# Optimization experiments

Hardware: AMD Instinct MI355X
Metric: run time of the kernel (lower is better)

## Reference

```python
import jax, jax.numpy as jnp
import numpy as np

B, C_IN, L, NCLASS = 256, 6, 512, 10

def setup_inputs() -> dict:
    key = jax.random.key(0)
    ks = jax.random.split(key, 16)
    g = lambda k, shp, s=0.05: jax.random.normal(k, shp, dtype=jnp.float32) * s
    return {
        "x": jax.random.normal(ks[0], (B, C_IN, L), dtype=jnp.float32),
        "conv1_w": g(ks[1], (32, C_IN, 3)),
        "conv1_b": g(ks[2], (32,)),
        "bn1_g": jnp.ones((32,), jnp.float32),
        "bn1_b": jnp.zeros((32,), jnp.float32),
        "bn1_m": g(ks[3], (32,)),
        "bn1_v": jnp.abs(g(ks[4], (32,))) + 1.0,
        "conv2_w": g(ks[5], (64, 32, 3)),
        "conv2_b": g(ks[6], (64,)),
        "bn2_g": jnp.ones((64,), jnp.float32),
        "bn2_b": jnp.zeros((64,), jnp.float32),
        "bn2_m": g(ks[7], (64,)),
        "bn2_v": jnp.abs(g(ks[8], (64,))) + 1.0,
        "wq": g(ks[9], (64, 64)),
        "bq": g(ks[10], (64,)),
        "wk": g(ks[11], (64, 64)),
        "bk": g(ks[12], (64,)),
        "wv": g(ks[13], (64, 64)),
        "bv": g(ks[14], (64,)),
        "fc_w": g(ks[15], (NCLASS, 64)),
        "fc_b": jnp.zeros((NCLASS,), jnp.float32),
    }

def _conv1d(x, w, b):
    # x: [B, C, L], w: [O, C, 3], padding=1 -> same length
    y = jax.lax.conv_general_dilated(
        x, w, window_strides=(1,), padding=[(1, 1)],
        dimension_numbers=("NCH", "OIH", "NCH"))
    return y + b[None, :, None]

def _bn(x, g, b, m, v, eps=1e-5):
    # eval-mode BatchNorm1d over channel dim of [B, C, L]
    inv = g * jax.lax.rsqrt(v + eps)
    return x * inv[None, :, None] + (b - m * inv)[None, :, None]

def reference(x, conv1_w, conv1_b, bn1_g, bn1_b, bn1_m, bn1_v,
              conv2_w, conv2_b, bn2_g, bn2_b, bn2_m, bn2_v,
              wq, bq, wk, bk, wv, bv, fc_w, fc_b):
    h = jax.nn.relu(_bn(_conv1d(x, conv1_w, conv1_b), bn1_g, bn1_b, bn1_m, bn1_v))
    h = jax.nn.relu(_bn(_conv1d(h, conv2_w, conv2_b), bn2_g, bn2_b, bn2_m, bn2_v))
    h = h.transpose(0, 2, 1)                      # [B, L, 64]
    q = h @ wq.T + bq
    k = h @ wk.T + bk
    v = h @ wv.T + bv
    scores = jnp.einsum("bqd,bkd->bqk", q, k) / jnp.sqrt(jnp.float32(64.0))
    attn = jax.nn.softmax(scores, axis=-1)
    out = jnp.einsum("bqk,bkd->bqd", attn, v)     # [B, L, 64]
    pooled = out.mean(axis=1)                     # [B, 64]
    return pooled @ fc_w.T + fc_b                 # [B, n_class]
```

## Files before the change

### kernel.cpp

```cpp
#include <hip/hip_runtime.h>
#include <hip/hip_bf16.h>


#define NB 256
#define LL 512
#define CIN 6
#define NCLASS 10
#define SLAB 8192
#define QSC 0.18033688f

typedef __bf16 bf16x8 __attribute__((ext_vector_type(8)));
typedef float f32x4 __attribute__((ext_vector_type(4)));
typedef unsigned short us4 __attribute__((ext_vector_type(4)));
typedef unsigned short us8 __attribute__((ext_vector_type(8)));
typedef unsigned int u32x4 __attribute__((ext_vector_type(4)));

static __device__ __forceinline__ unsigned short f2b(float f) {
    __bf16 h = (__bf16)f;
    return __builtin_bit_cast(unsigned short, h);
}

__global__ __launch_bounds__(256) void prep_weights(
    const float* __restrict__ w1, const float* __restrict__ cb1,
    const float* __restrict__ g1, const float* __restrict__ be1,
    const float* __restrict__ m1, const float* __restrict__ v1,
    const float* __restrict__ w2, const float* __restrict__ cb2,
    const float* __restrict__ g2, const float* __restrict__ be2,
    const float* __restrict__ m2, const float* __restrict__ v2,
    const float* __restrict__ wq, const float* __restrict__ wk,
    const float* __restrict__ wv,
    unsigned short* __restrict__ w1p, float* __restrict__ b1f,
    unsigned short* __restrict__ w2p, float* __restrict__ b2f,
    unsigned short* __restrict__ wqp, unsigned short* __restrict__ wkp,
    unsigned short* __restrict__ wvp)
{
    const int t = threadIdx.x;
    for (int idx = t; idx < 1024; idx += 256) {
        int c = idx >> 5, k = idx & 31;
        int dl = k >> 3, ci = k & 7;
        float inv = g1[c] * rsqrtf(v1[c] + 1e-5f);
        float val = (dl < 3 && ci < 6) ? w1[c * 18 + ci * 3 + dl] * inv : 0.f;
        w1p[idx] = f2b(val);
    }
    if (t < 32) {
        float inv = g1[t] * rsqrtf(v1[t] + 1e-5f);
        b1f[t] = be1[t] + (cb1[t] - m1[t]) * inv;
    }
    for (int idx = t; idx < 2048; idx += 256) {
        int c2 = idx >> 5, ci = idx & 31;
        float inv = g2[c2] * rsqrtf(v2[c2] + 1e-5f);
        const float* wp = w2 + c2 * 96 + ci * 3;
        w2p[c2 * 96 +      ci] = f2b(wp[0] * inv);
        w2p[c2 * 96 + 32 + ci] = f2b(wp[1] * inv);
        w2p[c2 * 96 + 64 + ci] = f2b(wp[2] * inv);
    }
    if (t >= 64 && t < 128) {
        int c2 = t - 64;
        float inv = g2[c2] * rsqrtf(v2[c2] + 1e-5f);
        b2f[c2] = be2[c2] + (cb2[c2] - m2[c2]) * inv;
    }
    for (int idx = t; idx < 4096; idx += 256) {
        int d = idx >> 6, k = idx & 63;
        int kc = k >> 5, quad = (k >> 3) & 3, e = k & 7;
        int ch = kc * 32 + (e >> 2) * 16 + quad * 4 + (e & 3);
        wqp[idx] = f2b(wq[d * 64 + ch] * QSC);
        wkp[idx] = f2b(wk[d * 64 + ch]);
        wvp[idx] = f2b(wv[d * 64 + ch]);
    }
}

__global__ __launch_bounds__(1024, 4) void fused_all(
    const float* __restrict__ x,
    const unsigned short* __restrict__ w1p, const float* __restrict__ b1f,
    const unsigned short* __restrict__ w2p, const float* __restrict__ b2f,
    const unsigned short* __restrict__ wqp, const unsigned short* __restrict__ wkp,
    const unsigned short* __restrict__ wvp,
    const float* __restrict__ bq, const float* __restrict__ bk,
    const float* __restrict__ bvp,
    const float* __restrict__ fcw, const float* __restrict__ fcb,
    float* __restrict__ outp)
{
    const int b = blockIdx.x;
    const int t = threadIdx.x;
    const int w = t >> 6, lane = t & 63, quad = lane >> 4, lc = lane & 15;

    __shared__ __align__(16) char smem[16 * SLAB + 8192];
    char* myslab = smem + w * SLAB;
    unsigned short* h1sl = (unsigned short*)myslab;
    unsigned short* Kf   = (unsigned short*)myslab;
    unsigned short* Vf   = (unsigned short*)(myslab + 4096);
    unsigned short* xstage = (unsigned short*)(smem + 16 * SLAB);
    float* redw   = (float*)(smem + 16 * SLAB) + w * 64;
    float* pooled = (float*)(smem + 16 * SLAB + 4096);

    if (t < 512) {
        us8 pk;
        #pragma unroll
        for (int ci = 0; ci < 6; ci++)
            pk[ci] = f2b(x[((size_t)b * CIN + ci) * LL + t]);
        pk[6] = 0; pk[7] = 0;
        *(us8*)&xstage[t * 8] = pk;
    }
    __syncthreads();

    bf16x8 bW1[2];
    #pragma unroll
    for (int nt = 0; nt < 2; nt++)
        bW1[nt] = *(const bf16x8*)(w1p + (nt * 16 + lc) * 32 + quad * 8);
    f32x4 b1q[2];
    #pragma unroll
    for (int nt = 0; nt < 2; nt++)
        b1q[nt] = *(const f32x4*)&b1f[nt * 16 + quad * 4];
    #pragma unroll
    for (int mt = 0; mt < 3; mt++) {
        int j = mt * 16 + lc;
        int P = w * 32 - 1 + j;
        int src = P + quad - 1;
        bool okx = (src >= 0) && (src < LL);
        int srcc = src < 0 ? 0 : (src > 511 ? 511 : src);
        u32x4 xv = *(const u32x4*)&xstage[srcc * 8];
        if (!okx) { xv[0] = 0u; xv[1] = 0u; xv[2] = 0u; xv[3] = 0u; }
        bf16x8 aX = __builtin_bit_cast(bf16x8, xv);
        bool pv = (P >= 0) && (P < LL);
        #pragma unroll
        for (int nt = 0; nt < 2; nt++) {
            f32x4 z = {0.f, 0.f, 0.f, 0.f};
            f32x4 h = __builtin_amdgcn_mfma_f32_16x16x32_bf16(bW1[nt], aX, z, 0, 0, 0);
            us4 pk;
            #pragma unroll
            for (int r = 0; r < 4; r++) {
                float y = h[r] + b1q[nt][r];
                y = (pv && y > 0.f) ? y : 0.f;
                pk[r] = f2b(y);
            }
            if (j < 34)
                *(us4*)&h1sl[j * 40 + nt * 16 + quad * 4] = pk;
        }
    }

    bf16x8 bX[2][3], aW2[4][3];
    #pragma unroll
    for (int rt = 0; rt < 2; rt++)
        #pragma unroll
        for (int kc = 0; kc < 3; kc++)
            bX[rt][kc] = *(const bf16x8*)&h1sl[(rt * 16 + lc + kc) * 40 + quad * 8];
    #pragma unroll
    for (int nt = 0; nt < 4; nt++)
        #pragma unroll
        for (int kc = 0; kc < 3; kc++)
            aW2[nt][kc] = *(const bf16x8*)(w2p + (nt * 16 + lc) * 96 + kc * 32 + quad * 8);

    f32x4 acc2[4][2];
    #pragma unroll
    for (int nt = 0; nt < 4; nt++)
        #pragma unroll
        for (int rt = 0; rt < 2; rt++) {
            f32x4 a = {0.f, 0.f, 0.f, 0.f};
            a = __builtin_amdgcn_mfma_f32_16x16x32_bf16(aW2[nt][0], bX[rt][0], a, 0, 0, 0);
            a = __builtin_amdgcn_mfma_f32_16x16x32_bf16(aW2[nt][1], bX[rt][1], a, 0, 0, 0);
            acc2[nt][rt] = __builtin_amdgcn_mfma_f32_16x16x32_bf16(aW2[nt][2], bX[rt][2], a, 0, 0, 0);
        }

    bf16x8 aH[2][2];
    #pragma unroll
    for (int nt2 = 0; nt2 < 4; nt2++) {
        f32x4 bb2 = *(const f32x4*)&b2f[nt2 * 16 + quad * 4];
        #pragma unroll
        for (int rt = 0; rt < 2; rt++)
            #pragma unroll
            for (int reg = 0; reg < 4; reg++) {
                float y = acc2[nt2][rt][reg] + bb2[reg];
                aH[rt][nt2 >> 1][(nt2 & 1) * 4 + reg] = (__bf16)(y > 0.f ? y : 0.f);
            }
    }

    bf16x8 aQ[2][2];
    {
        f32x4 Cq[4][2], bbq[4];
        #pragma unroll
        for (int nt = 0; nt < 4; nt++) {
            bf16x8 aW0 = *(const bf16x8*)(wqp + (nt * 16 + lc) * 64 + quad * 8);
            bf16x8 aW1 = *(const bf16x8*)(wqp + (nt * 16 + lc) * 64 + 32 + quad * 8);
            bbq[nt] = *(const f32x4*)&bq[nt * 16 + quad * 4];
            #pragma unroll
            for (int rt = 0; rt < 2; rt++) {
                f32x4 a = {0.f, 0.f, 0.f, 0.f};
                a = __builtin_amdgcn_mfma_f32_16x16x32_bf16(aW0, aH[rt][0], a, 0, 0, 0);
                Cq[nt][rt] = __builtin_amdgcn_mfma_f32_16x16x32_bf16(aW1, aH[rt][1], a, 0, 0, 0);
            }
        }
        #pragma unroll
        for (int rt = 0; rt < 2; rt++)
            #pragma unroll
            for (int nt = 0; nt < 4; nt++)
                #pragma unroll
                for (int reg = 0; reg < 4; reg++)
                    aQ[rt][nt >> 1][(nt & 1) * 4 + reg] =
                        (__bf16)(Cq[nt][rt][reg] + bbq[nt][reg] * QSC);
    }
    {
        f32x4 Ck[4][2], bbk[4];
        #pragma unroll
        for (int nt = 0; nt < 4; nt++) {
            bf16x8 aW0 = *(const bf16x8*)(wkp + (nt * 16 + lc) * 64 + quad * 8);
            bf16x8 aW1 = *(const bf16x8*)(wkp + (nt * 16 + lc) * 64 + 32 + quad * 8);
            bbk[nt] = *(const f32x4*)&bk[nt * 16 + quad * 4];
            #pragma unroll
            for (int rt = 0; rt < 2; rt++) {
                f32x4 a = {0.f, 0.f, 0.f, 0.f};
                a = __builtin_amdgcn_mfma_f32_16x16x32_bf16(aW0, aH[rt][0], a, 0, 0, 0);
                Ck[nt][rt] = __builtin_amdgcn_mfma_f32_16x16x32_bf16(aW1, aH[rt][1], a, 0, 0, 0);
            }
        }
        #pragma unroll
        for (int rt = 0; rt < 2; rt++)
            #pragma unroll
            for (int kc = 0; kc < 2; kc++) {
                us8 pk;
                #pragma unroll
                for (int e = 0; e < 8; e++) {
                    int nt = kc * 2 + (e >> 2), reg = e & 3;
                    pk[e] = f2b(Ck[nt][rt][reg] + bbk[nt][reg]);
                }
                *(us8*)&Kf[((rt * 2 + kc) << 9) + lane * 8] = pk;
            }
    }

    #pragma unroll
    for (int nt = 0; nt < 4; nt++) {
        bf16x8 bW0 = *(const bf16x8*)(wvp + (nt * 16 + lc) * 64 + quad * 8);
        bf16x8 bW1 = *(const bf16x8*)(wvp + (nt * 16 + lc) * 64 + 32 + quad * 8);
        const float bvv = bvp[nt * 16 + lc];
        f32x4 a0, a1;
        {
            f32x4 z = {0.f, 0.f, 0.f, 0.f};
            z = __builtin_amdgcn_mfma_f32_16x16x32_bf16(aH[0][0], bW0, z, 0, 0, 0);
            a0 = __builtin_amdgcn_mfma_f32_16x16x32_bf16(aH[0][1], bW1, z, 0, 0, 0);
        }
        {
            f32x4 z = {0.f, 0.f, 0.f, 0.f};
            z = __builtin_amdgcn_mfma_f32_16x16x32_bf16(aH[1][0], bW0, z, 0, 0, 0);
            a1 = __builtin_amdgcn_mfma_f32_16x16x32_bf16(aH[1][1], bW1, z, 0, 0, 0);
        }
        us8 pk;
        #pragma unroll
        for (int reg = 0; reg < 4; reg++) {
            pk[reg]     = f2b(a0[reg] + bvv);
            pk[4 + reg] = f2b(a1[reg] + bvv);
        }
        *(us8*)&Vf[nt * 512 + lane * 8] = pk;
    }

    __syncthreads();

    f32x4 outacc[2][4];
    #pragma unroll
    for (int rt = 0; rt < 2; rt++)
        #pragma unroll
        for (int dt = 0; dt < 4; dt++) outacc[rt][dt] = (f32x4){0.f, 0.f, 0.f, 0.f};
    float den[2] = {0.f, 0.f};

    bf16x8 bK2[2][2];
    {
        const unsigned short* sK = (const unsigned short*)smem;
        #pragma unroll
        for (int nt = 0; nt < 2; nt++)
            #pragma unroll
            for (int kc = 0; kc < 2; kc++)
                bK2[nt][kc] = *(const bf16x8*)&sK[((nt * 2 + kc) << 9) + lane * 8];
    }
    f32x4 sv[2][2];
    #pragma unroll
    for (int nt = 0; nt < 2; nt++)
        #pragma unroll
        for (int rt = 0; rt < 2; rt++) {
            f32x4 z = {0.f, 0.f, 0.f, 0.f};
            z = __builtin_amdgcn_mfma_f32_16x16x32_bf16(bK2[nt][0], aQ[rt][0], z, 0, 0, 0);
            sv[nt][rt] = __builtin_amdgcn_mfma_f32_16x16x32_bf16(bK2[nt][1], aQ[rt][1], z, 0, 0, 0);
        }

    for (int cc = 0; cc < 16; cc++) {
        const unsigned short* sV = (const unsigned short*)(smem + cc * SLAB + 4096);
        bf16x8 bV[4];
        #pragma unroll
        for (int dt = 0; dt < 4; dt++)
            bV[dt] = *(const bf16x8*)&sV[dt * 512 + lane * 8];
        if (cc < 15) {
            const unsigned short* sKn = (const unsigned short*)(smem + (cc + 1) * SLAB);
            #pragma unroll
            for (int nt = 0; nt < 2; nt++)
                #pragma unroll
                for (int kc = 0; kc < 2; kc++)
                    bK2[nt][kc] = *(const bf16x8*)&sKn[((nt * 2 + kc) << 9) + lane * 8];
        }
        bf16x8 aP[2];
        #pragma unroll
        for (int rt = 0; rt < 2; rt++)
            #pragma unroll
            for (int nt = 0; nt < 2; nt++)
                #pragma unroll
                for (int reg = 0; reg < 4; reg++) {
                    float p = __builtin_amdgcn_exp2f(sv[nt][rt][reg]);
                    den[rt] += p;
                    aP[rt][nt * 4 + reg] = (__bf16)p;
                }
        __builtin_amdgcn_s_setprio(1);
        #pragma unroll
        for (int dt = 0; dt < 4; dt++) {
            outacc[0][dt] = __builtin_amdgcn_mfma_f32_16x16x32_bf16(aP[0], bV[dt], outacc[0][dt], 0, 0, 0);
            outacc[1][dt] = __builtin_amdgcn_mfma_f32_16x16x32_bf16(aP[1], bV[dt], outacc[1][dt], 0, 0, 0);
        }
        if (cc < 15) {
            #pragma unroll
            for (int nt = 0; nt < 2; nt++)
                #pragma unroll
                for (int rt = 0; rt < 2; rt++) {
                    f32x4 z = {0.f, 0.f, 0.f, 0.f};
                    z = __builtin_amdgcn_mfma_f32_16x16x32_bf16(bK2[nt][0], aQ[rt][0], z, 0, 0, 0);
                    sv[nt][rt] = __builtin_amdgcn_mfma_f32_16x16x32_bf16(bK2[nt][1], aQ[rt][1], z, 0, 0, 0);
                }
        }
        __builtin_amdgcn_s_setprio(0);
    }

    float rden[2][4];
    #pragma unroll
    for (int rt = 0; rt < 2; rt++) {
        float d2 = den[rt];
        d2 += __shfl_xor(d2, 16);
        d2 += __shfl_xor(d2, 32);
        d2 = 1.0f / d2;
        #pragma unroll
        for (int reg = 0; reg < 4; reg++)
            rden[rt][reg] = __shfl(d2, quad * 4 + reg);
    }
    #pragma unroll
    for (int dt = 0; dt < 4; dt++) {
        float ps = 0.f;
        #pragma unroll
        for (int rt = 0; rt < 2; rt++)
            #pragma unroll
            for (int reg = 0; reg < 4; reg++)
                ps += outacc[rt][dt][reg] * rden[rt][reg];
        ps += __shfl_xor(ps, 16);
        ps += __shfl_xor(ps, 32);
        if (quad == 0) redw[dt * 16 + lc] = ps;
    }
    __syncthreads();
    if (t < 64) {
        float s = 0.f;
        #pragma unroll
        for (int ww = 0; ww < 16; ww++)
            s += *(const float*)(smem + 16 * SLAB + ww * 256 + t * 4);
        pooled[t] = s * (1.0f / 512.0f);
    }
    __syncthreads();
    if (t < NCLASS) {
        float acc = fcb[t];
        #pragma unroll
        for (int d = 0; d < 64; d++) acc += pooled[d] * fcw[t * 64 + d];
        outp[b * NCLASS + t] = acc;
    }
}

extern "C" void kernel_launch(void* const* d_in, const int* in_sizes, int n_in,
                              void* d_out, int out_size, void* d_ws, size_t ws_size,
                              hipStream_t stream)
{
    const float* x   = (const float*)d_in[0];
    const float* w1  = (const float*)d_in[1];
    const float* cb1 = (const float*)d_in[2];
    const float* g1  = (const float*)d_in[3];
    const float* be1 = (const float*)d_in[4];
    const float* m1  = (const float*)d_in[5];
    const float* v1  = (const float*)d_in[6];
    const float* w2  = (const float*)d_in[7];
    const float* cb2 = (const float*)d_in[8];
    const float* g2  = (const float*)d_in[9];
    const float* be2 = (const float*)d_in[10];
    const float* m2  = (const float*)d_in[11];
    const float* v2  = (const float*)d_in[12];
    const float* wq  = (const float*)d_in[13];
    const float* bq  = (const float*)d_in[14];
    const float* wk  = (const float*)d_in[15];
    const float* bk  = (const float*)d_in[16];
    const float* wv  = (const float*)d_in[17];
    const float* bv  = (const float*)d_in[18];
    const float* fcw = (const float*)d_in[19];
    const float* fcb = (const float*)d_in[20];
    float* out = (float*)d_out;

    char* ws = (char*)d_ws;
    unsigned short* w1p = (unsigned short*)(ws);
    float*          b1f = (float*)(ws + 2048u);
    float*          b2f = (float*)(ws + 2176u);
    unsigned short* w2p = (unsigned short*)(ws + 2432u);
    unsigned short* wqp = (unsigned short*)(ws + 14720u);
    unsigned short* wkp = (unsigned short*)(ws + 22912u);
    unsigned short* wvp = (unsigned short*)(ws + 31104u);

    prep_weights<<<dim3(1), 256, 0, stream>>>(w1, cb1, g1, be1, m1, v1,
                                              w2, cb2, g2, be2, m2, v2,
                                              wq, wk, wv,
                                              w1p, b1f, w2p, b2f, wqp, wkp, wvp);
    fused_all<<<dim3(NB), 1024, 0, stream>>>(x, w1p, b1f, w2p, b2f,
                                             wqp, wkp, wvp,
                                             bq, bk, bv, fcw, fcb, out);
}
```

Baseline: 130.0 us.

## Halve block to 512 threads with each wave owning two query tiles

```diff
diff --git a/kernel.cpp b/kernel.cpp
--- a/kernel.cpp
+++ b/kernel.cpp
@@ -34,19 +34,19 @@
     unsigned short* __restrict__ wqp, unsigned short* __restrict__ wkp,
     unsigned short* __restrict__ wvp)
 {
-    const int t = threadIdx.x;
-    for (int idx = t; idx < 1024; idx += 256) {
+    const int tt = blockIdx.x * 256 + threadIdx.x;
+    for (int idx = tt; idx < 1024; idx += 2048) {
         int c = idx >> 5, k = idx & 31;
         int dl = k >> 3, ci = k & 7;
         float inv = g1[c] * rsqrtf(v1[c] + 1e-5f);
         float val = (dl < 3 && ci < 6) ? w1[c * 18 + ci * 3 + dl] * inv : 0.f;
         w1p[idx] = f2b(val);
     }
-    if (t < 32) {
-        float inv = g1[t] * rsqrtf(v1[t] + 1e-5f);
-        b1f[t] = be1[t] + (cb1[t] - m1[t]) * inv;
-    }
-    for (int idx = t; idx < 2048; idx += 256) {
+    if (tt < 32) {
+        float inv = g1[tt] * rsqrtf(v1[tt] + 1e-5f);
+        b1f[tt] = be1[tt] + (cb1[tt] - m1[tt]) * inv;
+    }
+    for (int idx = tt; idx < 2048; idx += 2048) {
         int c2 = idx >> 5, ci = idx & 31;
         float inv = g2[c2] * rsqrtf(v2[c2] + 1e-5f);
         const float* wp = w2 + c2 * 96 + ci * 3;
@@ -54,12 +54,12 @@
         w2p[c2 * 96 + 32 + ci] = f2b(wp[1] * inv);
         w2p[c2 * 96 + 64 + ci] = f2b(wp[2] * inv);
     }
-    if (t >= 64 && t < 128) {
-        int c2 = t - 64;
+    if (tt >= 64 && tt < 128) {
+        int c2 = tt - 64;
         float inv = g2[c2] * rsqrtf(v2[c2] + 1e-5f);
         b2f[c2] = be2[c2] + (cb2[c2] - m2[c2]) * inv;
     }
-    for (int idx = t; idx < 4096; idx += 256) {
+    for (int idx = tt; idx < 4096; idx += 2048) {
         int d = idx >> 6, k = idx & 63;
         int kc = k >> 5, quad = (k >> 3) & 3, e = k & 7;
         int ch = kc * 32 + (e >> 2) * 16 + quad * 4 + (e & 3);
@@ -69,7 +69,7 @@
     }
 }
 
-__global__ __launch_bounds__(1024, 4) void fused_all(
+__global__ __launch_bounds__(512, 2) void fused_all(
     const float* __restrict__ x,
     const unsigned short* __restrict__ w1p, const float* __restrict__ b1f,
     const unsigned short* __restrict__ w2p, const float* __restrict__ b2f,
@@ -85,15 +85,11 @@
     const int w = t >> 6, lane = t & 63, quad = lane >> 4, lc = lane & 15;
 
     __shared__ __align__(16) char smem[16 * SLAB + 8192];
-    char* myslab = smem + w * SLAB;
-    unsigned short* h1sl = (unsigned short*)myslab;
-    unsigned short* Kf   = (unsigned short*)myslab;
-    unsigned short* Vf   = (unsigned short*)(myslab + 4096);
     unsigned short* xstage = (unsigned short*)(smem + 16 * SLAB);
     float* redw   = (float*)(smem + 16 * SLAB) + w * 64;
     float* pooled = (float*)(smem + 16 * SLAB + 4096);
 
-    if (t < 512) {
+    {
         us8 pk;
         #pragma unroll
         for (int ci = 0; ci < 6; ci++)
@@ -103,162 +99,171 @@
     }
     __syncthreads();
 
-    bf16x8 bW1[2];
+    bf16x8 aQ4[4][2];
     #pragma unroll
-    for (int nt = 0; nt < 2; nt++)
-        bW1[nt] = *(const bf16x8*)(w1p + (nt * 16 + lc) * 32 + quad * 8);
-    f32x4 b1q[2];
-    #pragma unroll
-    for (int nt = 0; nt < 2; nt++)
-        b1q[nt] = *(const f32x4*)&b1f[nt * 16 + quad * 4];
-    #pragma unroll
-    for (int mt = 0; mt < 3; mt++) {
-        int j = mt * 16 + lc;
-        int P = w * 32 - 1 + j;
-        int src = P + quad - 1;
-        bool okx = (src >= 0) && (src < LL);
-        int srcc = src < 0 ? 0 : (src > 511 ? 511 : src);
-        u32x4 xv = *(const u32x4*)&xstage[srcc * 8];
-        if (!okx) { xv[0] = 0u; xv[1] = 0u; xv[2] = 0u; xv[3] = 0u; }
-        bf16x8 aX = __builtin_bit_cast(bf16x8, xv);
-        bool pv = (P >= 0) && (P < LL);
-        #pragma unroll
-        for (int nt = 0; nt < 2; nt++) {
-            f32x4 z = {0.f, 0.f, 0.f, 0.f};
-            f32x4 h = __builtin_amdgcn_mfma_f32_16x16x32_bf16(bW1[nt], aX, z, 0, 0, 0);
-            us4 pk;
-            #pragma unroll
-            for (int r = 0; r < 4; r++) {
-                float y = h[r] + b1q[nt][r];
-                y = (pv && y > 0.f) ? y : 0.f;
-                pk[r] = f2b(y);
-            }
-            if (j < 34)
-                *(us4*)&h1sl[j * 40 + nt * 16 + quad * 4] = pk;
-        }
-    }
-
-    bf16x8 bX[2][3], aW2[4][3];
-    #pragma unroll
-    for (int rt = 0; rt < 2; rt++)
-        #pragma unroll
-        for (int kc = 0; kc < 3; kc++)
-            bX[rt][kc] = *(const bf16x8*)&h1sl[(rt * 16 + lc + kc) * 40 + quad * 8];
-    #pragma unroll
-    for (int nt = 0; nt < 4; nt++)
-        #pragma unroll
-        for (int kc = 0; kc < 3; kc++)
-            aW2[nt][kc] = *(const bf16x8*)(w2p + (nt * 16 + lc) * 96 + kc * 32 + quad * 8);
-
-    f32x4 acc2[4][2];
-    #pragma unroll
-    for (int nt = 0; nt < 4; nt++)
-        #pragma unroll
-        for (int rt = 0; rt < 2; rt++) {
-            f32x4 a = {0.f, 0.f, 0.f, 0.f};
-            a = __builtin_amdgcn_mfma_f32_16x16x32_bf16(aW2[nt][0], bX[rt][0], a, 0, 0, 0);
-            a = __builtin_amdgcn_mfma_f32_16x16x32_bf16(aW2[nt][1], bX[rt][1], a, 0, 0, 0);
-            acc2[nt][rt] = __builtin_amdgcn_mfma_f32_16x16x32_bf16(aW2[nt][2], bX[rt][2], a, 0, 0, 0);
-        }
-
-    bf16x8 aH[2][2];
-    #pragma unroll
-    for (int nt2 = 0; nt2 < 4; nt2++) {
-        f32x4 bb2 = *(const f32x4*)&b2f[nt2 * 16 + quad * 4];
+    for (int sg = 0; sg < 2; sg++) {
+        const int g = 2 * w + sg;
+        char* gslab = smem + g * SLAB;
+        unsigned short* h1sl = (unsigned short*)gslab;
+        unsigned short* Kf   = (unsigned short*)gslab;
+        unsigned short* Vf   = (unsigned short*)(gslab + 4096);
+
+        bf16x8 bW1[2];
+        #pragma unroll
+        for (int nt = 0; nt < 2; nt++)
+            bW1[nt] = *(const bf16x8*)(w1p + (nt * 16 + lc) * 32 + quad * 8);
+        f32x4 b1q[2];
+        #pragma unroll
+        for (int nt = 0; nt < 2; nt++)
+            b1q[nt] = *(const f32x4*)&b1f[nt * 16 + quad * 4];
+        #pragma unroll
+        for (int mt = 0; mt < 3; mt++) {
+            int j = mt * 16 + lc;
+            int P = g * 32 - 1 + j;
+            int src = P + quad - 1;
+            bool okx = (src >= 0) && (src < LL);
+            int srcc = src < 0 ? 0 : (src > 511 ? 511 : src);
+            u32x4 xv = *(const u32x4*)&xstage[srcc * 8];
+            if (!okx) { xv[0] = 0u; xv[1] = 0u; xv[2] = 0u; xv[3] = 0u; }
+            bf16x8 aX = __builtin_bit_cast(bf16x8, xv);
+            bool pv = (P >= 0) && (P < LL);
+            #pragma unroll
+            for (int nt = 0; nt < 2; nt++) {
+                f32x4 z = {0.f, 0.f, 0.f, 0.f};
+                f32x4 h = __builtin_amdgcn_mfma_f32_16x16x32_bf16(bW1[nt], aX, z, 0, 0, 0);
+                us4 pk;
+                #pragma unroll
+                for (int r = 0; r < 4; r++) {
+                    float y = h[r] + b1q[nt][r];
+                    y = (pv && y > 0.f) ? y : 0.f;
+                    pk[r] = f2b(y);
+                }
+                if (j < 34)
+                    *(us4*)&h1sl[j * 40 + nt * 16 + quad * 4] = pk;
+            }
+        }
+
+        bf16x8 bX[2][3], aW2[4][3];
         #pragma unroll
         for (int rt = 0; rt < 2; rt++)
             #pragma unroll
-            for (int reg = 0; reg < 4; reg++) {
-                float y = acc2[nt2][rt][reg] + bb2[reg];
-                aH[rt][nt2 >> 1][(nt2 & 1) * 4 + reg] = (__bf16)(y > 0.f ? y : 0.f);
-            }
-    }
-
-    bf16x8 aQ[2][2];
-    {
-        f32x4 Cq[4][2], bbq[4];
-        #pragma unroll
-        for (int nt = 0; nt < 4; nt++) {
-            bf16x8 aW0 = *(const bf16x8*)(wqp + (nt * 16 + lc) * 64 + quad * 8);
-            bf16x8 aW1 = *(const bf16x8*)(wqp + (nt * 16 + lc) * 64 + 32 + quad * 8);
-            bbq[nt] = *(const f32x4*)&bq[nt * 16 + quad * 4];
+            for (int kc = 0; kc < 3; kc++)
+                bX[rt][kc] = *(const bf16x8*)&h1sl[(rt * 16 + lc + kc) * 40 + quad * 8];
+        #pragma unroll
+        for (int nt = 0; nt < 4; nt++)
+            #pragma unroll
+            for (int kc = 0; kc < 3; kc++)
+                aW2[nt][kc] = *(const bf16x8*)(w2p + (nt * 16 + lc) * 96 + kc * 32 + quad * 8);
+
+        f32x4 acc2[4][2];
+        #pragma unroll
+        for (int nt = 0; nt < 4; nt++)
             #pragma unroll
             for (int rt = 0; rt < 2; rt++) {
                 f32x4 a = {0.f, 0.f, 0.f, 0.f};
-                a = __builtin_amdgcn_mfma_f32_16x16x32_bf16(aW0, aH[rt][0], a, 0, 0, 0);
-                Cq[nt][rt] = __builtin_amdgcn_mfma_f32_16x16x32_bf16(aW1, aH[rt][1], a, 0, 0, 0);
-            }
-        }
-        #pragma unroll
-        for (int rt = 0; rt < 2; rt++)
-            #pragma unroll
-            for (int nt = 0; nt < 4; nt++)
-                #pragma unroll
-                for (int reg = 0; reg < 4; reg++)
-                    aQ[rt][nt >> 1][(nt & 1) * 4 + reg] =
-                        (__bf16)(Cq[nt][rt][reg] + bbq[nt][reg] * QSC);
-    }
-    {
-        f32x4 Ck[4][2], bbk[4];
+                a = __builtin_amdgcn_mfma_f32_16x16x32_bf16(aW2[nt][0], bX[rt][0], a, 0, 0, 0);
+                a = __builtin_amdgcn_mfma_f32_16x16x32_bf16(aW2[nt][1], bX[rt][1], a, 0, 0, 0);
+                acc2[nt][rt] = __builtin_amdgcn_mfma_f32_16x16x32_bf16(aW2[nt][2], bX[rt][2], a, 0, 0, 0);
+            }
+
+        bf16x8 aH[2][2];
+        #pragma unroll
+        for (int nt2 = 0; nt2 < 4; nt2++) {
+            f32x4 bb2 = *(const f32x4*)&b2f[nt2 * 16 + quad * 4];
+            #pragma unroll
+            for (int rt = 0; rt < 2; rt++)
+                #pragma unroll
+                for (int reg = 0; reg < 4; reg++) {
+                    float y = acc2[nt2][rt][reg] + bb2[reg];
+                    aH[rt][nt2 >> 1][(nt2 & 1) * 4 + reg] = (__bf16)(y > 0.f ? y : 0.f);
+                }
+        }
+
+        {
+            f32x4 Cq[4][2], bbq[4];
+            #pragma unroll
+            for (int nt = 0; nt < 4; nt++) {
+                bf16x8 aW0 = *(const bf16x8*)(wqp + (nt * 16 + lc) * 64 + quad * 8);
+                bf16x8 aW1 = *(const bf16x8*)(wqp + (nt * 16 + lc) * 64 + 32 + quad * 8);
+                bbq[nt] = *(const f32x4*)&bq[nt * 16 + quad * 4];
+                #pragma unroll
+                for (int rt = 0; rt < 2; rt++) {
+                    f32x4 a = {0.f, 0.f, 0.f, 0.f};
+                    a = __builtin_amdgcn_mfma_f32_16x16x32_bf16(aW0, aH[rt][0], a, 0, 0, 0);
+                    Cq[nt][rt] = __builtin_amdgcn_mfma_f32_16x16x32_bf16(aW1, aH[rt][1], a, 0, 0, 0);
+                }
+            }
+            #pragma unroll
+            for (int rt = 0; rt < 2; rt++)
+                #pragma unroll
+                for (int nt = 0; nt < 4; nt++)
+                    #pragma unroll
+                    for (int reg = 0; reg < 4; reg++)
+                        aQ4[sg * 2 + rt][nt >> 1][(nt & 1) * 4 + reg] =
+                            (__bf16)(Cq[nt][rt][reg] + bbq[nt][reg] * QSC);
+        }
+        {
+            f32x4 Ck[4][2], bbk[4];
+            #pragma unroll
+            for (int nt = 0; nt < 4; nt++) {
+                bf16x8 aW0 = *(const bf16x8*)(wkp + (nt * 16 + lc) * 64 + quad * 8);
+                bf16x8 aW1 = *(const bf16x8*)(wkp + (nt * 16 + lc) * 64 + 32 + quad * 8);
+                bbk[nt] = *(const f32x4*)&bk[nt * 16 + quad * 4];
+                #pragma unroll
+                for (int rt = 0; rt < 2; rt++) {
+                    f32x4 a = {0.f, 0.f, 0.f, 0.f};
+                    a = __builtin_amdgcn_mfma_f32_16x16x32_bf16(aW0, aH[rt][0], a, 0, 0, 0);
+                    Ck[nt][rt] = __builtin_amdgcn_mfma_f32_16x16x32_bf16(aW1, aH[rt][1], a, 0, 0, 0);
+                }
+            }
+            #pragma unroll
+            for (int rt = 0; rt < 2; rt++)
+                #pragma unroll
+                for (int kc = 0; kc < 2; kc++) {
+                    us8 pk;
+                    #pragma unroll
+                    for (int e = 0; e < 8; e++) {
+                        int nt = kc * 2 + (e >> 2), reg = e & 3;
+                        pk[e] = f2b(Ck[nt][rt][reg] + bbk[nt][reg]);
+                    }
+                    *(us8*)&Kf[((rt * 2 + kc) << 9) + lane * 8] = pk;
+                }
+        }
+
         #pragma unroll
         for (int nt = 0; nt < 4; nt++) {
-            bf16x8 aW0 = *(const bf16x8*)(wkp + (nt * 16 + lc) * 64 + quad * 8);
-            bf16x8 aW1 = *(const bf16x8*)(wkp + (nt * 16 + lc) * 64 + 32 + quad * 8);
-            bbk[nt] = *(const f32x4*)&bk[nt * 16 + quad * 4];
-            #pragma unroll
-            for (int rt = 0; rt < 2; rt++) {
-                f32x4 a = {0.f, 0.f, 0.f, 0.f};
-                a = __builtin_amdgcn_mfma_f32_16x16x32_bf16(aW0, aH[rt][0], a, 0, 0, 0);
-                Ck[nt][rt] = __builtin_amdgcn_mfma_f32_16x16x32_bf16(aW1, aH[rt][1], a, 0, 0, 0);
-            }
-        }
-        #pragma unroll
-        for (int rt = 0; rt < 2; rt++)
-            #pragma unroll
-            for (int kc = 0; kc < 2; kc++) {
-                us8 pk;
-                #pragma unroll
-                for (int e = 0; e < 8; e++) {
-                    int nt = kc * 2 + (e >> 2), reg = e & 3;
-                    pk[e] = f2b(Ck[nt][rt][reg] + bbk[nt][reg]);
-                }
-                *(us8*)&Kf[((rt * 2 + kc) << 9) + lane * 8] = pk;
-            }
-    }
-
+            bf16x8 bW0 = *(const bf16x8*)(wvp + (nt * 16 + lc) * 64 + quad * 8);
+            bf16x8 bW1 = *(const bf16x8*)(wvp + (nt * 16 + lc) * 64 + 32 + quad * 8);
+            const float bvv = bvp[nt * 16 + lc];
+            f32x4 a0, a1;
+            {
+                f32x4 z = {0.f, 0.f, 0.f, 0.f};
+                z = __builtin_amdgcn_mfma_f32_16x16x32_bf16(aH[0][0], bW0, z, 0, 0, 0);
+                a0 = __builtin_amdgcn_mfma_f32_16x16x32_bf16(aH[0][1], bW1, z, 0, 0, 0);
+            }
+            {
+                f32x4 z = {0.f, 0.f, 0.f, 0.f};
+                z = __builtin_amdgcn_mfma_f32_16x16x32_bf16(aH[1][0], bW0, z, 0, 0, 0);
+                a1 = __builtin_amdgcn_mfma_f32_16x16x32_bf16(aH[1][1], bW1, z, 0, 0, 0);
+            }
+            us8 pk;
+            #pragma unroll
+            for (int reg = 0; reg < 4; reg++) {
+                pk[reg]     = f2b(a0[reg] + bvv);
+                pk[4 + reg] = f2b(a1[reg] + bvv);
+            }
+            *(us8*)&Vf[nt * 512 + lane * 8] = pk;
+        }
+    }
+
+    __syncthreads();
+
+    f32x4 outacc[4][4];
     #pragma unroll
-    for (int nt = 0; nt < 4; nt++) {
-        bf16x8 bW0 = *(const bf16x8*)(wvp + (nt * 16 + lc) * 64 + quad * 8);
-        bf16x8 bW1 = *(const bf16x8*)(wvp + (nt * 16 + lc) * 64 + 32 + quad * 8);
-        const float bvv = bvp[nt * 16 + lc];
-        f32x4 a0, a1;
-        {
-            f32x4 z = {0.f, 0.f, 0.f, 0.f};
-            z = __builtin_amdgcn_mfma_f32_16x16x32_bf16(aH[0][0], bW0, z, 0, 0, 0);
-            a0 = __builtin_amdgcn_mfma_f32_16x16x32_bf16(aH[0][1], bW1, z, 0, 0, 0);
-        }
-        {
-            f32x4 z = {0.f, 0.f, 0.f, 0.f};
-            z = __builtin_amdgcn_mfma_f32_16x16x32_bf16(aH[1][0], bW0, z, 0, 0, 0);
-            a1 = __builtin_amdgcn_mfma_f32_16x16x32_bf16(aH[1][1], bW1, z, 0, 0, 0);
-        }
-        us8 pk;
-        #pragma unroll
-        for (int reg = 0; reg < 4; reg++) {
-            pk[reg]     = f2b(a0[reg] + bvv);
-            pk[4 + reg] = f2b(a1[reg] + bvv);
-        }
-        *(us8*)&Vf[nt * 512 + lane * 8] = pk;
-    }
-
-    __syncthreads();
-
-    f32x4 outacc[2][4];
-    #pragma unroll
-    for (int rt = 0; rt < 2; rt++)
+    for (int rt = 0; rt < 4; rt++)
         #pragma unroll
         for (int dt = 0; dt < 4; dt++) outacc[rt][dt] = (f32x4){0.f, 0.f, 0.f, 0.f};
-    float den[2] = {0.f, 0.f};
+    float den[4] = {0.f, 0.f, 0.f, 0.f};
 
     bf16x8 bK2[2][2];
     {
@@ -269,14 +274,14 @@
             for (int kc = 0; kc < 2; kc++)
                 bK2[nt][kc] = *(const bf16x8*)&sK[((nt * 2 + kc) << 9) + lane * 8];
     }
-    f32x4 sv[2][2];
+    f32x4 sv[2][4];
     #pragma unroll
     for (int nt = 0; nt < 2; nt++)
         #pragma unroll
-        for (int rt = 0; rt < 2; rt++) {
+        for (int rt = 0; rt < 4; rt++) {
             f32x4 z = {0.f, 0.f, 0.f, 0.f};
-            z = __builtin_amdgcn_mfma_f32_16x16x32_bf16(bK2[nt][0], aQ[rt][0], z, 0, 0, 0);
-            sv[nt][rt] = __builtin_amdgcn_mfma_f32_16x16x32_bf16(bK2[nt][1], aQ[rt][1], z, 0, 0, 0);
+            z = __builtin_amdgcn_mfma_f32_16x16x32_bf16(bK2[nt][0], aQ4[rt][0], z, 0, 0, 0);
+            sv[nt][rt] = __builtin_amdgcn_mfma_f32_16x16x32_bf16(bK2[nt][1], aQ4[rt][1], z, 0, 0, 0);
         }
 
     for (int cc = 0; cc < 16; cc++) {
@@ -293,9 +298,9 @@
                 for (int kc = 0; kc < 2; kc++)
                     bK2[nt][kc] = *(const bf16x8*)&sKn[((nt * 2 + kc) << 9) + lane * 8];
         }
-        bf16x8 aP[2];
-        #pragma unroll
-        for (int rt = 0; rt < 2; rt++)
+        bf16x8 aP[4];
+        #pragma unroll
+        for (int rt = 0; rt < 4; rt++)
             #pragma unroll
             for (int nt = 0; nt < 2; nt++)
                 #pragma unroll
@@ -306,26 +311,26 @@
                 }
         __builtin_amdgcn_s_setprio(1);
         #pragma unroll
-        for (int dt = 0; dt < 4; dt++) {
-            outacc[0][dt] = __builtin_amdgcn_mfma_f32_16x16x32_bf16(aP[0], bV[dt], outacc[0][dt], 0, 0, 0);
-            outacc[1][dt] = __builtin_amdgcn_mfma_f32_16x16x32_bf16(aP[1], bV[dt], outacc[1][dt], 0, 0, 0);
-        }
+        for (int rt = 0; rt < 4; rt++)
+            #pragma unroll
+            for (int dt = 0; dt < 4; dt++)
+                outacc[rt][dt] = __builtin_amdgcn_mfma_f32_16x16x32_bf16(aP[rt], bV[dt], outacc[rt][dt], 0, 0, 0);
         if (cc < 15) {
             #pragma unroll
             for (int nt = 0; nt < 2; nt++)
                 #pragma unroll
-                for (int rt = 0; rt < 2; rt++) {
+                for (int rt = 0; rt < 4; rt++) {
                     f32x4 z = {0.f, 0.f, 0.f, 0.f};
-                    z = __builtin_amdgcn_mfma_f32_16x16x32_bf16(bK2[nt][0], aQ[rt][0], z, 0, 0, 0);
-                    sv[nt][rt] = __builtin_amdgcn_mfma_f32_16x16x32_bf16(bK2[nt][1], aQ[rt][1], z, 0, 0, 0);
+                    z = __builtin_amdgcn_mfma_f32_16x16x32_bf16(bK2[nt][0], aQ4[rt][0], z, 0, 0, 0);
+                    sv[nt][rt] = __builtin_amdgcn_mfma_f32_16x16x32_bf16(bK2[nt][1], aQ4[rt][1], z, 0, 0, 0);
                 }
         }
         __builtin_amdgcn_s_setprio(0);
     }
 
-    float rden[2][4];
+    float rden[4][4];
     #pragma unroll
-    for (int rt = 0; rt < 2; rt++) {
+    for (int rt = 0; rt < 4; rt++) {
         float d2 = den[rt];
         d2 += __shfl_xor(d2, 16);
         d2 += __shfl_xor(d2, 32);
@@ -338,7 +343,7 @@
     for (int dt = 0; dt < 4; dt++) {
         float ps = 0.f;
         #pragma unroll
-        for (int rt = 0; rt < 2; rt++)
+        for (int rt = 0; rt < 4; rt++)
             #pragma unroll
             for (int reg = 0; reg < 4; reg++)
                 ps += outacc[rt][dt][reg] * rden[rt][reg];
@@ -350,7 +355,7 @@
     if (t < 64) {
         float s = 0.f;
         #pragma unroll
-        for (int ww = 0; ww < 16; ww++)
+        for (int ww = 0; ww < 8; ww++)
             s += *(const float*)(smem + 16 * SLAB + ww * 256 + t * 4);
         pooled[t] = s * (1.0f / 512.0f);
     }
@@ -399,11 +404,11 @@
     unsigned short* wkp = (unsigned short*)(ws + 22912u);
     unsigned short* wvp = (unsigned short*)(ws + 31104u);
 
-    prep_weights<<<dim3(1), 256, 0, stream>>>(w1, cb1, g1, be1, m1, v1,
+    prep_weights<<<dim3(8), 256, 0, stream>>>(w1, cb1, g1, be1, m1, v1,
                                               w2, cb2, g2, be2, m2, v2,
                                               wq, wk, wv,
                                               w1p, b1f, w2p, b2f, wqp, wkp, wvp);
-    fused_all<<<dim3(NB), 1024, 0, stream>>>(x, w1p, b1f, w2p, b2f,
-                                             wqp, wkp, wvp,
-                                             bq, bk, bv, fcw, fcb, out);
+    fused_all<<<dim3(NB), 512, 0, stream>>>(x, w1p, b1f, w2p, b2f,
+                                            wqp, wkp, wvp,
+                                            bq, bk, bv, fcw, fcb, out);
 }
```

After: 124.2 us. -4.5%, faster.
